# Optimization experiments

Measured on AMD Instinct MI355X. Metric: run time of the kernel, lower is better.

Reference implementation:

```python
import jax, jax.numpy as jnp
import numpy as np

B, T = 64, 1024
EMB = 10          # embedding_dim
H = 64            # hidden_size
NH = 2            # attention heads
IN = 3 * EMB      # 30 = GRU input_size
GAMMA = 1.0


def rbf(d):
    # BondExpansionRBF: exp(-gamma * |center - d|^2), centers = 1..10
    centers = jnp.arange(1, EMB + 1, dtype=d.dtype)          # [10]
    return jnp.exp(-GAMMA * (centers - d[..., None]) ** 2)   # [..., 10]


def gru_layer(x, w_ih, w_hh, b_ih, b_hh):
    # x: [B,T,D] -> [B,T,H]; torch GRU gate order: r, z, n
    Bn = x.shape[0]
    Hn = w_hh.shape[1]
    xw = jnp.einsum('btd,gd->btg', x, w_ih) + b_ih           # [B,T,3H] precomputed input proj

    def step(h, xt):
        gh = h @ w_hh.T + b_hh
        xr, xz, xn = jnp.split(xt, 3, axis=-1)
        hr, hz, hn = jnp.split(gh, 3, axis=-1)
        r = jax.nn.sigmoid(xr + hr)
        z = jax.nn.sigmoid(xz + hz)
        n = jnp.tanh(xn + r * hn)
        h = (1.0 - z) * n + z * h
        return h, h

    _, ys = jax.lax.scan(step, jnp.zeros((Bn, Hn), x.dtype), jnp.swapaxes(xw, 0, 1))
    return jnp.swapaxes(ys, 0, 1)


def mha(x, in_w, in_b, out_w, out_b):
    # torch nn.MultiheadAttention (batch_first, self-attn), eval mode
    Bn, Tn, E = x.shape
    Hd = E // NH
    qkv = x @ in_w.T + in_b                                   # [B,T,3E]
    q, k, v = jnp.split(qkv, 3, axis=-1)

    def heads(t):
        return t.reshape(Bn, Tn, NH, Hd).transpose(0, 2, 1, 3)  # [B,NH,T,Hd]

    q, k, v = heads(q), heads(k), heads(v)
    scores = jnp.einsum('bhqd,bhkd->bhqk', q, k) / jnp.asarray(np.sqrt(Hd), x.dtype)
    a = jax.nn.softmax(scores, axis=-1)
    o = jnp.einsum('bhqk,bhkd->bhqd', a, v).transpose(0, 2, 1, 3).reshape(Bn, Tn, E)
    return o @ out_w.T + out_b


def forward(atom_idx, bond_dist, emb, w_ih0, w_hh0, b_ih0, b_hh0,
            w_ih1, w_hh1, b_ih1, b_hh1, in_w1, in_b1, out_w1, out_b1,
            in_w2, in_b2, out_w2, out_b2, w_l, b_l, w_l1, b_l1):
    idx_i = atom_idx[..., 0]
    idx_j = atom_idx[..., 1]
    # index 0 -> zero vector (padding semantics of the python-loop conditionals)
    e_i = jnp.where((idx_i != 0)[..., None], emb[idx_i], 0.0)   # [B,T,10]
    e_j = jnp.where((idx_j != 0)[..., None], emb[idx_j], 0.0)   # [B,T,10]
    d = jnp.where((idx_i != 0)[..., None], rbf(bond_dist), 0.0)  # [B,T,10]
    x = jnp.concatenate([e_i, e_j, d], axis=-1)                  # [B,T,30]

    g = gru_layer(x, w_ih0, w_hh0, b_ih0, b_hh0)
    g = gru_layer(g, w_ih1, w_hh1, b_ih1, b_hh1)
    a = mha(g, in_w1, in_b1, out_w1, out_b1)
    a = mha(a, in_w2, in_b2, out_w2, out_b2)

    last = a[:, -1, :]                                           # [B,H]
    h = jax.nn.relu(last @ w_l.T + b_l)                          # [B,32]
    out = h @ w_l1.T + b_l1                                      # [B,1]
    return out[:, 0]                                             # [B]


def setup_inputs() -> dict:
    key = jax.random.key(0)
    ks = jax.random.split(key, 20)

    def n(k, shape, s=0.05):
        return jax.random.normal(k, shape, jnp.float32) * s

    return {
        'atom_idx': jax.random.randint(ks[0], (B, T, 2), 0, 119),
        'bond_dist': jax.random.uniform(ks[1], (B, T), jnp.float32) * 10.0,
        'emb': n(ks[2], (119, EMB), 1.0),
        'w_ih0': n(ks[3], (3 * H, IN)), 'w_hh0': n(ks[4], (3 * H, H)),
        'b_ih0': n(ks[5], (3 * H,)), 'b_hh0': n(ks[6], (3 * H,)),
        'w_ih1': n(ks[7], (3 * H, H)), 'w_hh1': n(ks[8], (3 * H, H)),
        'b_ih1': n(ks[9], (3 * H,)), 'b_hh1': n(ks[10], (3 * H,)),
        'in_w1': n(ks[11], (3 * H, H)), 'in_b1': n(ks[12], (3 * H,)),
        'out_w1': n(ks[13], (H, H)), 'out_b1': jnp.zeros((H,), jnp.float32),
        'in_w2': n(ks[14], (3 * H, H)), 'in_b2': n(ks[15], (3 * H,)),
        'out_w2': n(ks[16], (H, H)), 'out_b2': jnp.zeros((H,), jnp.float32),
        'w_l': n(ks[17], (32, H)), 'b_l': jnp.zeros((32,), jnp.float32),
        'w_l1': n(ks[18], (1, 32)), 'b_l1': jnp.zeros((1,), jnp.float32),
    }


def reference(atom_idx, bond_dist, emb, w_ih0, w_hh0, b_ih0, b_hh0,
              w_ih1, w_hh1, b_ih1, b_hh1, in_w1, in_b1, out_w1, out_b1,
              in_w2, in_b2, out_w2, out_b2, w_l, b_l, w_l1, b_l1):
    return forward(atom_idx, bond_dist, emb, w_ih0, w_hh0, b_ih0, b_hh0,
                   w_ih1, w_hh1, b_ih1, b_hh1, in_w1, in_b1, out_w1, out_b1,
                   in_w2, in_b2, out_w2, out_b2, w_l, b_l, w_l1, b_l1)
```

## Files before the change

### kernel.cpp

```cpp
#include <hip/hip_runtime.h>

typedef unsigned int uint_t;
typedef float v2f __attribute__((ext_vector_type(2)));

#define BB 64
#define TT 1024

__device__ __forceinline__ float sigm(float x) { return 1.f / (1.f + __expf(-x)); }
__device__ __forceinline__ float tanh_f(float x) { float e = __expf(2.f * x); return 1.f - 2.f / (e + 1.f); }
__device__ __forceinline__ int finitef(float x) { return (x == x) && (fabsf(x) < 1e30f); }

__device__ __forceinline__ void spinwait(volatile int* f, int v) {
  if (*f >= v) { asm volatile("" ::: "memory"); return; }
  int it = 0;
  while (*f < v && it < (1 << 15)) { __builtin_amdgcn_s_sleep(1); ++it; }
  asm volatile("" ::: "memory");
}

__device__ __forceinline__ float feat(int b, int t, int j,
                                      const int* atom_idx, const float* bond_dist,
                                      const float* emb) {
  int ii = atom_idx[(b * TT + t) * 2 + 0];
  if (j < 10) {
    return ii ? emb[ii * 10 + j] : 0.f;
  } else if (j < 20) {
    int jj = atom_idx[(b * TT + t) * 2 + 1];
    return jj ? emb[jj * 10 + (j - 10)] : 0.f;
  } else {
    float d = bond_dist[b * TT + t];
    float c = (float)(j - 19);
    float df = c - d;
    return ii ? __expf(-df * df) : 0.f;
  }
}

extern "C" __global__ void __launch_bounds__(256)
k_xw0(const int* atom_idx, const float* bond_dist, const float* emb,
      const float* w_ih0, const float* b_ih0, float* xw0) {
  int b  = blockIdx.x >> 4;
  int t0 = (blockIdx.x & 15) << 6;
  int tid = threadIdx.x;
  __shared__ float xt[64 * 31];
  for (int i = tid; i < 64 * 30; i += 256) {
    int r = i / 30, j = i % 30;
    xt[r * 31 + j] = feat(b, t0 + r, j, atom_idx, bond_dist, emb);
  }
  __syncthreads();
  int r = tid & 63, gq = tid >> 6;
  const float* ar = &xt[r * 31];
  for (int g0 = gq * 8; g0 < 192; g0 += 32) {
    float acc[8];
    #pragma unroll
    for (int j = 0; j < 8; ++j) acc[j] = b_ih0[g0 + j];
    #pragma unroll
    for (int c = 0; c < 30; ++c) {
      float a = ar[c];
      #pragma unroll
      for (int j = 0; j < 8; ++j) acc[j] += a * w_ih0[(g0 + j) * 30 + c];
    }
    #pragma unroll
    for (int j = 0; j < 8; ++j)
      xw0[((size_t)b * TT + t0 + r) * 192 + g0 + j] = acc[j];
  }
}

__device__ __forceinline__ void gemm64b(const float* __restrict__ act_g,
                                        const float* __restrict__ w,
                                        const float* __restrict__ bias,
                                        float* al,
                                        int G, int tid,
                                        float* out, int out_rstride, size_t out_base) {
  for (int i = tid; i < 64 * 64; i += 256) {
    int r = i >> 6, c = i & 63;
    al[r * 65 + c] = act_g[r * 64 + c];
  }
  __syncthreads();
  int r = tid & 63, gq = tid >> 6;
  const float* ar = &al[r * 65];
  for (int g0 = gq * 8; g0 < G; g0 += 32) {
    float acc[8];
    #pragma unroll
    for (int j = 0; j < 8; ++j) acc[j] = bias[g0 + j];
    #pragma unroll
    for (int c = 0; c < 64; ++c) {
      float a = ar[c];
      #pragma unroll
      for (int j = 0; j < 8; ++j) acc[j] += a * w[(size_t)(g0 + j) * 64 + c];
    }
    #pragma unroll
    for (int j = 0; j < 8; ++j)
      out[out_base + (size_t)r * out_rstride + g0 + j] = acc[j];
  }
}

__device__ __forceinline__ void loadw2(const float* p, v2f* w2) {
  const float4* p4 = (const float4*)p;
  #pragma unroll
  for (int i = 0; i < 16; ++i) {
    float4 a = p4[i];
    v2f lo; lo.x = a.x; lo.y = a.y;
    v2f hi; hi.x = a.z; hi.y = a.w;
    w2[2 * i] = lo; w2[2 * i + 1] = hi;
  }
}

extern "C" __global__ void __launch_bounds__(192, 1)
k_grufused(const float* xw0, const float* w_hh0, const float* b_hh0,
           const float* w_ih1, const float* b_ih1,
           const float* w_hh1, const float* b_hh1, float* g1out) {
  int b    = blockIdx.x;
  int lane = threadIdx.x & 63;
  int wid  = threadIdx.x >> 6;
  __shared__ __align__(16) float h0ring[16][64];
  __shared__ __align__(16) float xwring[16][192];
  __shared__ __align__(16) float h1pp[2][64];
  __shared__ int flags[3];

  if (threadIdx.x < 3) flags[threadIdx.x] = -1;
  if (wid == 0) h0ring[15][lane] = 0.f;
  if (wid == 2) h1pp[0][lane] = 0.f;
  __syncthreads();

  volatile int* w0d = &flags[0];
  volatile int* w1d = &flags[1];
  volatile int* w2d = &flags[2];

  if (wid == 0) {
    v2f wr2[32], wz2[32], wn2[32];
    loadw2(w_hh0 + (size_t)lane * 64,        wr2);
    loadw2(w_hh0 + (size_t)(64 + lane) * 64, wz2);
    loadw2(w_hh0 + (size_t)(128 + lane) * 64, wn2);
    float br = b_hh0[lane], bz = b_hh0[64 + lane], bn = b_hh0[128 + lane];
    float hv = 0.f;
    const float* xwb = xw0 + (size_t)b * TT * 192;
    float xr0 = xwb[      lane], xz0 = xwb[ 64 + lane], xn0 = xwb[128 + lane];
    float xr1 = xwb[192 + lane], xz1 = xwb[256 + lane], xn1 = xwb[320 + lane];
    float xr2 = xwb[384 + lane], xz2 = xwb[448 + lane], xn2 = xwb[512 + lane];
    float xr3 = xwb[576 + lane], xz3 = xwb[640 + lane], xn3 = xwb[704 + lane];

    auto gstep = [&](int s, float xr, float xz, float xn) {
      const float4* hp4 = (const float4*)h0ring[(s + 15) & 15];
      v2f ar; ar.x = br; ar.y = 0.f;
      v2f az; az.x = bz; az.y = 0.f;
      v2f an; an.x = bn; an.y = 0.f;
      #pragma unroll
      for (int i = 0; i < 16; ++i) {
        float4 h4 = hp4[i];
        v2f hlo; hlo.x = h4.x; hlo.y = h4.y;
        v2f hhi; hhi.x = h4.z; hhi.y = h4.w;
        ar += wr2[2*i] * hlo; ar += wr2[2*i+1] * hhi;
        az += wz2[2*i] * hlo; az += wz2[2*i+1] * hhi;
        an += wn2[2*i] * hlo; an += wn2[2*i+1] * hhi;
      }
      float r = sigm(xr + (ar.x + ar.y));
      float z = sigm(xz + (az.x + az.y));
      float n = tanh_f(xn + r * (an.x + an.y));
      hv = (1.f - z) * n + z * hv;
      h0ring[s & 15][lane] = hv;
    };
    auto pf = [&](int s, float& a, float& bb_, float& c) {
      const float* xp = xwb + (size_t)s * 192;
      a = xp[lane]; bb_ = xp[64 + lane]; c = xp[128 + lane];
    };

    for (int s0 = 0; s0 < TT; s0 += 4) {
      if (s0 >= 16) spinwait(w1d, s0 - 13);
      bool dopf = (s0 < TT - 4);
      gstep(s0 + 0, xr0, xz0, xn0); if (dopf) pf(s0 + 4, xr0, xz0, xn0);
      gstep(s0 + 1, xr1, xz1, xn1); if (dopf) pf(s0 + 5, xr1, xz1, xn1);
      gstep(s0 + 2, xr2, xz2, xn2); if (dopf) pf(s0 + 6, xr2, xz2, xn2);
      gstep(s0 + 3, xr3, xz3, xn3); if (dopf) pf(s0 + 7, xr3, xz3, xn3);
      asm volatile("" ::: "memory");
      if (lane == 0) *w0d = s0 + 3;
    }
  } else if (wid == 1) {
    v2f wr2[32], wz2[32], wn2[32];
    loadw2(w_ih1 + (size_t)lane * 64,        wr2);
    loadw2(w_ih1 + (size_t)(64 + lane) * 64, wz2);
    loadw2(w_ih1 + (size_t)(128 + lane) * 64, wn2);
    float br = b_ih1[lane], bz = b_ih1[64 + lane], bn = b_ih1[128 + lane];

    for (int t0 = 0; t0 < TT; t0 += 4) {
      spinwait(w0d, t0 + 3);
      if (t0 >= 16) spinwait(w2d, t0 - 13);
      #pragma unroll
      for (int k = 0; k < 4; ++k) {
        int t = t0 + k;
        const float4* hp4 = (const float4*)h0ring[t & 15];
        v2f ar; ar.x = br; ar.y = 0.f;
        v2f az; az.x = bz; az.y = 0.f;
        v2f an; an.x = bn; an.y = 0.f;
        #pragma unroll
        for (int i = 0; i < 16; ++i) {
          float4 h4 = hp4[i];
          v2f hlo; hlo.x = h4.x; hlo.y = h4.y;
          v2f hhi; hhi.x = h4.z; hhi.y = h4.w;
          ar += wr2[2*i] * hlo; ar += wr2[2*i+1] * hhi;
          az += wz2[2*i] * hlo; az += wz2[2*i+1] * hhi;
          an += wn2[2*i] * hlo; an += wn2[2*i+1] * hhi;
        }
        xwring[t & 15][lane]       = ar.x + ar.y;
        xwring[t & 15][64 + lane]  = az.x + az.y;
        xwring[t & 15][128 + lane] = an.x + an.y;
      }
      asm volatile("" ::: "memory");
      if (lane == 0) *w1d = t0 + 3;
    }
  } else {
    v2f wr2[32], wz2[32], wn2[32];
    loadw2(w_hh1 + (size_t)lane * 64,        wr2);
    loadw2(w_hh1 + (size_t)(64 + lane) * 64, wz2);
    loadw2(w_hh1 + (size_t)(128 + lane) * 64, wn2);
    float br = b_hh1[lane], bz = b_hh1[64 + lane], bn = b_hh1[128 + lane];
    float hv = 0.f;
    float* houtb = g1out + (size_t)b * TT * 64 + lane;

    for (int t0 = 0; t0 < TT; t0 += 4) {
      spinwait(w1d, t0 + 3);
      #pragma unroll
      for (int k = 0; k < 4; ++k) {
        int t = t0 + k;
        float xr = xwring[t & 15][lane];
        float xz = xwring[t & 15][64 + lane];
        float xn = xwring[t & 15][128 + lane];
        const float4* hp4 = (const float4*)h1pp[t & 1];
        v2f ar; ar.x = br; ar.y = 0.f;
        v2f az; az.x = bz; az.y = 0.f;
        v2f an; an.x = bn; an.y = 0.f;
        #pragma unroll
        for (int i = 0; i < 16; ++i) {
          float4 h4 = hp4[i];
          v2f hlo; hlo.x = h4.x; hlo.y = h4.y;
          v2f hhi; hhi.x = h4.z; hhi.y = h4.w;
          ar += wr2[2*i] * hlo; ar += wr2[2*i+1] * hhi;
          az += wz2[2*i] * hlo; az += wz2[2*i+1] * hhi;
          an += wn2[2*i] * hlo; an += wn2[2*i+1] * hhi;
        }
        float r = sigm(xr + (ar.x + ar.y));
        float z = sigm(xz + (az.x + az.y));
        float n = tanh_f(xn + r * (an.x + an.y));
        hv = (1.f - z) * n + z * hv;
        h1pp[(t + 1) & 1][lane] = hv;
        houtb[(size_t)t * 64] = hv;
      }
      asm volatile("" ::: "memory");
      if (lane == 0) *w2d = t0 + 3;
    }
  }
}

extern "C" __global__ void __launch_bounds__(256)
k_qkv(const float* g1, const float* in_w1, const float* in_b1,
      float* q1, float* k1, float* v1) {
  int b  = blockIdx.x >> 4;
  int t0 = (blockIdx.x & 15) << 6;
  int tid = threadIdx.x;
  __shared__ float al[64 * 65];
  const float* act = g1 + ((size_t)b * TT + t0) * 64;
  for (int i = tid; i < 64 * 64; i += 256) {
    int r = i >> 6, c = i & 63;
    al[r * 65 + c] = act[r * 64 + c];
  }
  __syncthreads();
  int r = tid & 63, gq = tid >> 6;
  const float* ar = &al[r * 65];
  for (int g0 = gq * 8; g0 < 192; g0 += 32) {
    float acc[8];
    #pragma unroll
    for (int j = 0; j < 8; ++j) acc[j] = in_b1[g0 + j];
    #pragma unroll
    for (int c = 0; c < 64; ++c) {
      float a = ar[c];
      #pragma unroll
      for (int j = 0; j < 8; ++j) acc[j] += a * in_w1[(size_t)(g0 + j) * 64 + c];
    }
    int p = g0 / 64;
    float* outp = (p == 0) ? q1 : ((p == 1) ? k1 : v1);
    #pragma unroll
    for (int j = 0; j < 8; ++j) {
      int rem = (g0 - p * 64) + j;
      int hd = rem >> 5, d = rem & 31;
      outp[(((size_t)b * 2 + hd) * TT + t0 + r) * 32 + d] = acc[j];
    }
  }
}

extern "C" __global__ void __launch_bounds__(256, 2)
k_attn(const float* q1, const float* k1, const float* v1, float* po, float* ml) {
  int gid = blockIdx.x;
  int b   = gid >> 3;
  int h   = (gid >> 2) & 1;
  int seg = (gid >> 1) & 1;
  int qb  = gid & 1;
  int tid = threadIdx.x;
  int tq0 = qb * 512 + tid;
  __shared__ __align__(16) float Kt[64 * 32];
  __shared__ __align__(16) float Vt[64 * 32];
  v2f q2[32], o2[32];
  const float* qp0 = q1 + (((size_t)b * 2 + h) * TT + tq0) * 32;
  const float* qp1 = qp0 + 256 * 32;
  #pragma unroll
  for (int i = 0; i < 8; ++i) {
    float4 v0 = ((const float4*)qp0)[i];
    float4 v1r = ((const float4*)qp1)[i];
    q2[4*i+0] = (v2f){v0.x, v1r.x};
    q2[4*i+1] = (v2f){v0.y, v1r.y};
    q2[4*i+2] = (v2f){v0.z, v1r.z};
    q2[4*i+3] = (v2f){v0.w, v1r.w};
  }
  #pragma unroll
  for (int i = 0; i < 32; ++i) o2[i] = (v2f){0.f, 0.f};
  float m0 = -1e30f, l0 = 0.f, m1 = -1e30f, l1 = 0.f;
  const float scale = 0.17677669529663687f;
  const float4* kb = (const float4*)(k1 + ((size_t)b * 2 + h) * TT * 32);
  const float4* vb = (const float4*)(v1 + ((size_t)b * 2 + h) * TT * 32);
  int k0 = seg << 9;
  for (int kt = k0; kt < k0 + 512; kt += 64) {
    __syncthreads();
    ((float4*)Kt)[tid]       = kb[kt * 8 + tid];
    ((float4*)Kt)[tid + 256] = kb[kt * 8 + tid + 256];
    ((float4*)Vt)[tid]       = vb[kt * 8 + tid];
    ((float4*)Vt)[tid + 256] = vb[kt * 8 + tid + 256];
    __syncthreads();
    #pragma unroll 1
    for (int c0 = 0; c0 < 64; c0 += 8) {
      v2f sv2[8];
      #pragma unroll
      for (int j = 0; j < 8; ++j) {
        const float4* kr = (const float4*)&Kt[(c0 + j) * 32];
        v2f a0 = (v2f){0.f, 0.f}, a1 = (v2f){0.f, 0.f};
        #pragma unroll
        for (int i = 0; i < 8; ++i) {
          float4 kv = kr[i];
          a0 += q2[4*i+0] * (v2f){kv.x, kv.x};
          a1 += q2[4*i+1] * (v2f){kv.y, kv.y};
          a0 += q2[4*i+2] * (v2f){kv.z, kv.z};
          a1 += q2[4*i+3] * (v2f){kv.w, kv.w};
        }
        v2f s = a0 + a1;
        sv2[j] = (v2f){s.x * scale, s.y * scale};
      }
      float cm0 = sv2[0].x, cm1 = sv2[0].y;
      #pragma unroll
      for (int j = 1; j < 8; ++j) { cm0 = fmaxf(cm0, sv2[j].x); cm1 = fmaxf(cm1, sv2[j].y); }
      float mn0 = fmaxf(m0, cm0), mn1 = fmaxf(m1, cm1);
      float al0 = __expf(m0 - mn0), al1 = __expf(m1 - mn1);
      float ps0 = 0.f, ps1 = 0.f;
      #pragma unroll
      for (int j = 0; j < 8; ++j) {
        float e0 = __expf(sv2[j].x - mn0); ps0 += e0;
        float e1 = __expf(sv2[j].y - mn1); ps1 += e1;
        sv2[j] = (v2f){e0, e1};
      }
      l0 = l0 * al0 + ps0; m0 = mn0;
      l1 = l1 * al1 + ps1; m1 = mn1;
      v2f al2 = (v2f){al0, al1};
      #pragma unroll
      for (int i = 0; i < 8; ++i) {
        v2f A0 = o2[4*i+0] * al2;
        v2f A1 = o2[4*i+1] * al2;
        v2f A2 = o2[4*i+2] * al2;
        v2f A3 = o2[4*i+3] * al2;
        #pragma unroll
        for (int j = 0; j < 8; ++j) {
          float4 vv = *(const float4*)&Vt[(c0 + j) * 32 + 4 * i];
          A0 += sv2[j] * (v2f){vv.x, vv.x};
          A1 += sv2[j] * (v2f){vv.y, vv.y};
          A2 += sv2[j] * (v2f){vv.z, vv.z};
          A3 += sv2[j] * (v2f){vv.w, vv.w};
        }
        o2[4*i+0] = A0; o2[4*i+1] = A1; o2[4*i+2] = A2; o2[4*i+3] = A3;
      }
    }
  }
  size_t rb0 = (((size_t)(b * 2 + h)) * 2 + seg) * TT + tq0;
  size_t rb1 = rb0 + 256;
  float* op0 = po + rb0 * 32;
  float* op1 = po + rb1 * 32;
  #pragma unroll
  for (int i = 0; i < 8; ++i) {
    float4 s0; s0.x = o2[4*i+0].x; s0.y = o2[4*i+1].x; s0.z = o2[4*i+2].x; s0.w = o2[4*i+3].x;
    float4 s1; s1.x = o2[4*i+0].y; s1.y = o2[4*i+1].y; s1.z = o2[4*i+2].y; s1.w = o2[4*i+3].y;
    ((float4*)op0)[i] = s0;
    ((float4*)op1)[i] = s1;
  }
  ml[rb0 * 2 + 0] = m0; ml[rb0 * 2 + 1] = l0;
  ml[rb1 * 2 + 0] = m1; ml[rb1 * 2 + 1] = l1;
}

extern "C" __global__ void __launch_bounds__(256)
k_attn_comb(const float* po, const float* ml, float* attnO) {
  int row = blockIdx.x * 256 + threadIdx.x;
  int bh = row >> 10;
  int t  = row & 1023;
  int b = bh >> 1, h = bh & 1;
  size_t r0 = ((size_t)bh * 2 + 0) * TT + t;
  size_t r1 = ((size_t)bh * 2 + 1) * TT + t;
  float m0 = ml[r0 * 2], l0 = ml[r0 * 2 + 1];
  float m1 = ml[r1 * 2], l1 = ml[r1 * 2 + 1];
  float m = fmaxf(m0, m1);
  float w0 = __expf(m0 - m), w1 = __expf(m1 - m);
  float inv = 1.f / (w0 * l0 + w1 * l1);
  w0 *= inv; w1 *= inv;
  const float4* p0 = (const float4*)(po + r0 * 32);
  const float4* p1 = (const float4*)(po + r1 * 32);
  float* op = attnO + ((size_t)b * TT + t) * 64 + h * 32;
  #pragma unroll
  for (int i = 0; i < 8; ++i) {
    float4 a = p0[i], c = p1[i], r;
    r.x = a.x * w0 + c.x * w1; r.y = a.y * w0 + c.y * w1;
    r.z = a.z * w0 + c.z * w1; r.w = a.w * w0 + c.w * w1;
    ((float4*)op)[i] = r;
  }
}

extern "C" __global__ void __launch_bounds__(256)
k_oproj(const float* attnO, const float* out_w1, const float* out_b1, float* a1) {
  int b  = blockIdx.x >> 4;
  int t0 = (blockIdx.x & 15) << 6;
  __shared__ float al[64 * 65];
  gemm64b(attnO + ((size_t)b * TT + t0) * 64, out_w1, out_b1, al, 64, threadIdx.x,
          a1, 64, ((size_t)b * TT + t0) * 64);
}

extern "C" __global__ void __launch_bounds__(256)
k_mha2kv(const float* a1, const float* in_w2, const float* in_b2,
         float* s2, float* v2) {
  int b  = blockIdx.x >> 4;
  int t0 = (blockIdx.x & 15) << 6;
  int tid = threadIdx.x;
  __shared__ float a1r[64 * 65];
  __shared__ float q2s[64];
  __shared__ float alast[64];
  if (tid < 64) alast[tid] = a1[((size_t)b * TT + (TT - 1)) * 64 + tid];
  for (int i = tid; i < 4096; i += 256) {
    int r = i >> 6, e = i & 63;
    a1r[r * 65 + e] = a1[((size_t)b * TT + t0 + r) * 64 + e];
  }
  __syncthreads();
  if (tid < 64) {
    float acc = in_b2[tid];
    const float* wr = in_w2 + (size_t)tid * 64;
    #pragma unroll
    for (int e = 0; e < 64; ++e) acc += alast[e] * wr[e];
    q2s[tid] = acc;
  }
  __syncthreads();
  int tt = tid & 63;
  int role = tid >> 6;
  const float* ar = &a1r[tt * 65];
  const float scale = 0.17677669529663687f;
  if (role < 2) {
    float s = 0.f;
    for (int d = 0; d < 32; ++d) {
      int row = 64 + role * 32 + d;
      const float* wr = in_w2 + (size_t)row * 64;
      float acc = in_b2[row];
      #pragma unroll
      for (int e = 0; e < 64; ++e) acc += ar[e] * wr[e];
      s += q2s[row - 64] * acc;
    }
    s2[((size_t)b * 2 + role) * TT + t0 + tt] = s * scale;
  } else {
    int half = role - 2;
    for (int d = 0; d < 32; ++d) {
      int vd = half * 32 + d;
      int row = 128 + vd;
      const float* wr = in_w2 + (size_t)row * 64;
      float acc = in_b2[row];
      #pragma unroll
      for (int e = 0; e < 64; ++e) acc += ar[e] * wr[e];
      v2[((size_t)b * TT + t0 + tt) * 64 + vd] = acc;
    }
  }
}

extern "C" __global__ void __launch_bounds__(256)
k_final(const float* s2, const float* v2,
        const float* out_w2, const float* out_b2,
        const float* w_l, const float* b_l,
        const float* w_l1, const float* b_l1,
        float* out) {
  int b = blockIdx.x;
  int tid = threadIdx.x;
  __shared__ float sm[2 * 1024];
  __shared__ float red[8];
  __shared__ float invl[2];
  __shared__ float opart[4 * 64];
  __shared__ float of[64];
  __shared__ float a2[64];
  __shared__ float hbuf[32];
  __shared__ int bad;
  if (tid == 0) bad = 0;
  for (int i = tid; i < 2048; i += 256) sm[i] = s2[(size_t)b * 2 * TT + i];
  __syncthreads();
  int lane = tid & 63;
  int wid = tid >> 6;
  for (int hh = 0; hh < 2; ++hh) {
    float mx = -1e30f;
    for (int i = tid; i < 1024; i += 256) mx = fmaxf(mx, sm[hh * 1024 + i]);
    #pragma unroll
    for (int off = 32; off > 0; off >>= 1) mx = fmaxf(mx, __shfl_down(mx, off));
    if (lane == 0) red[wid] = mx;
    __syncthreads();
    if (tid == 0) red[4] = fmaxf(fmaxf(red[0], red[1]), fmaxf(red[2], red[3]));
    __syncthreads();
    mx = red[4];
    float s = 0.f;
    for (int i = tid; i < 1024; i += 256) {
      float e = __expf(sm[hh * 1024 + i] - mx);
      sm[hh * 1024 + i] = e;
      s += e;
    }
    #pragma unroll
    for (int off = 32; off > 0; off >>= 1) s += __shfl_down(s, off);
    if (lane == 0) red[wid] = s;
    __syncthreads();
    if (tid == 0) invl[hh] = 1.f / (red[0] + red[1] + red[2] + red[3]);
    __syncthreads();
  }
  {
    int dp = tid & 63;
    int part = tid >> 6;
    int hh = dp >> 5;
    float acc = 0.f;
    for (int t = part * 256; t < part * 256 + 256; ++t)
      acc += sm[hh * 1024 + t] * v2[((size_t)b * TT + t) * 64 + dp];
    opart[part * 64 + dp] = acc;
  }
  __syncthreads();
  if (tid < 64) {
    float o = (opart[tid] + opart[64 + tid] + opart[128 + tid] + opart[192 + tid]) * invl[tid >> 5];
    of[tid] = o;
    if (!finitef(o)) bad = 1;
  }
  __syncthreads();
  if (tid < 64) {
    float acc = out_b2[tid];
    const float* wr = out_w2 + (size_t)tid * 64;
    #pragma unroll
    for (int d = 0; d < 64; ++d) acc += of[d] * wr[d];
    a2[tid] = acc;
  }
  __syncthreads();
  if (tid < 32) {
    float acc = b_l[tid];
    const float* wr = w_l + (size_t)tid * 64;
    #pragma unroll
    for (int e = 0; e < 64; ++e) acc += a2[e] * wr[e];
    hbuf[tid] = fmaxf(acc, 0.f);
  }
  __syncthreads();
  if (tid == 0) {
    float acc = b_l1[0];
    #pragma unroll
    for (int j = 0; j < 32; ++j) acc += hbuf[j] * w_l1[j];
    out[b] = bad ? 777.0f : acc;
  }
}

extern "C" void kernel_launch(void* const* d_in, const int* in_sizes, int n_in,
                              void* d_out, int out_size, void* d_ws, size_t ws_size,
                              hipStream_t stream) {
  const int*   atom_idx  = (const int*)d_in[0];
  const float* bond_dist = (const float*)d_in[1];
  const float* emb       = (const float*)d_in[2];
  const float* w_ih0     = (const float*)d_in[3];
  const float* w_hh0     = (const float*)d_in[4];
  const float* b_ih0     = (const float*)d_in[5];
  const float* b_hh0     = (const float*)d_in[6];
  const float* w_ih1     = (const float*)d_in[7];
  const float* w_hh1     = (const float*)d_in[8];
  const float* b_ih1     = (const float*)d_in[9];
  const float* b_hh1     = (const float*)d_in[10];
  const float* in_w1     = (const float*)d_in[11];
  const float* in_b1     = (const float*)d_in[12];
  const float* out_w1    = (const float*)d_in[13];
  const float* out_b1    = (const float*)d_in[14];
  const float* in_w2     = (const float*)d_in[15];
  const float* in_b2     = (const float*)d_in[16];
  const float* out_w2    = (const float*)d_in[17];
  const float* out_b2    = (const float*)d_in[18];
  const float* w_l       = (const float*)d_in[19];
  const float* b_l       = (const float*)d_in[20];
  const float* w_l1      = (const float*)d_in[21];
  const float* b_l1      = (const float*)d_in[22];

  char* ws = (char*)d_ws;
  float* X  = (float*)(ws);
  float* A  = (float*)(ws + 50331648);
  float* Bq = (float*)(ws + 67108864);
  float* D  = (float*)(ws + 83886080);
  float* q1 = X;
  float* k1 = X + 4194304;
  float* v1 = X + 8388608;
  float* po = (float*)(ws + 16777216);
  float* ml = Bq;

  k_xw0      <<<dim3(1024), dim3(256), 0, stream>>>(atom_idx, bond_dist, emb, w_ih0, b_ih0, X);
  k_grufused <<<dim3(64),   dim3(192), 0, stream>>>(X, w_hh0, b_hh0, w_ih1, b_ih1, w_hh1, b_hh1, Bq);
  k_qkv      <<<dim3(1024), dim3(256), 0, stream>>>(Bq, in_w1, in_b1, q1, k1, v1);
  k_attn     <<<dim3(512),  dim3(256), 0, stream>>>(q1, k1, v1, po, ml);
  k_attn_comb<<<dim3(512),  dim3(256), 0, stream>>>(po, ml, A);
  k_oproj    <<<dim3(1024), dim3(256), 0, stream>>>(A, out_w1, out_b1, Bq);
  k_mha2kv   <<<dim3(1024), dim3(256), 0, stream>>>(Bq, in_w2, in_b2, D, X);
  k_final    <<<dim3(64),   dim3(256), 0, stream>>>(D, X, out_w2, out_b2, w_l, b_l, w_l1, b_l1, (float*)d_out);
}
```

Measured before the change: 1.301 ms.

## Process four query rows per thread in attention kernel to double K/V reuse

The attention kernel now assigns four query rows per thread instead of two and halves the grid, so each K/V tile loaded into shared memory is reused across twice as many queries. This cuts LDS reads and global K/V traffic per query. In exchange, per-thread register use roughly doubles, launch bounds drop to one block per SM, and there are fewer blocks to hide latency, risking spills or lower occupancy.

```diff
diff --git a/kernel.cpp b/kernel.cpp
--- a/kernel.cpp
+++ b/kernel.cpp
@@ -285,32 +285,34 @@
   }
 }
 
-extern "C" __global__ void __launch_bounds__(256, 2)
+extern "C" __global__ void __launch_bounds__(256, 1)
 k_attn(const float* q1, const float* k1, const float* v1, float* po, float* ml) {
   int gid = blockIdx.x;
-  int b   = gid >> 3;
-  int h   = (gid >> 2) & 1;
-  int seg = (gid >> 1) & 1;
-  int qb  = gid & 1;
+  int b   = gid >> 2;
+  int h   = (gid >> 1) & 1;
+  int seg = gid & 1;
   int tid = threadIdx.x;
-  int tq0 = qb * 512 + tid;
   __shared__ __align__(16) float Kt[64 * 32];
   __shared__ __align__(16) float Vt[64 * 32];
-  v2f q2[32], o2[32];
-  const float* qp0 = q1 + (((size_t)b * 2 + h) * TT + tq0) * 32;
-  const float* qp1 = qp0 + 256 * 32;
+  v2f qA[32], oA[32], qB[32], oB[32];
+  {
+    const float* p0 = q1 + (((size_t)b * 2 + h) * TT + tid) * 32;
+    #pragma unroll
+    for (int i = 0; i < 8; ++i) {
+      float4 a = ((const float4*)(p0))[i];
+      float4 c = ((const float4*)(p0 + 256 * 32))[i];
+      float4 d = ((const float4*)(p0 + 512 * 32))[i];
+      float4 e = ((const float4*)(p0 + 768 * 32))[i];
+      qA[4*i+0] = (v2f){a.x, c.x}; qA[4*i+1] = (v2f){a.y, c.y};
+      qA[4*i+2] = (v2f){a.z, c.z}; qA[4*i+3] = (v2f){a.w, c.w};
+      qB[4*i+0] = (v2f){d.x, e.x}; qB[4*i+1] = (v2f){d.y, e.y};
+      qB[4*i+2] = (v2f){d.z, e.z}; qB[4*i+3] = (v2f){d.w, e.w};
+    }
+  }
   #pragma unroll
-  for (int i = 0; i < 8; ++i) {
-    float4 v0 = ((const float4*)qp0)[i];
-    float4 v1r = ((const float4*)qp1)[i];
-    q2[4*i+0] = (v2f){v0.x, v1r.x};
-    q2[4*i+1] = (v2f){v0.y, v1r.y};
-    q2[4*i+2] = (v2f){v0.z, v1r.z};
-    q2[4*i+3] = (v2f){v0.w, v1r.w};
-  }
-  #pragma unroll
-  for (int i = 0; i < 32; ++i) o2[i] = (v2f){0.f, 0.f};
+  for (int i = 0; i < 32; ++i) { oA[i] = (v2f){0.f, 0.f}; oB[i] = (v2f){0.f, 0.f}; }
   float m0 = -1e30f, l0 = 0.f, m1 = -1e30f, l1 = 0.f;
+  float m2 = -1e30f, l2 = 0.f, m3 = -1e30f, l3 = 0.f;
   const float scale = 0.17677669529663687f;
   const float4* kb = (const float4*)(k1 + ((size_t)b * 2 + h) * TT * 32);
   const float4* vb = (const float4*)(v1 + ((size_t)b * 2 + h) * TT * 32);
@@ -324,68 +326,90 @@
     __syncthreads();
     #pragma unroll 1
     for (int c0 = 0; c0 < 64; c0 += 8) {
-      v2f sv2[8];
+      v2f svA[8], svB[8];
       #pragma unroll
       for (int j = 0; j < 8; ++j) {
         const float4* kr = (const float4*)&Kt[(c0 + j) * 32];
-        v2f a0 = (v2f){0.f, 0.f}, a1 = (v2f){0.f, 0.f};
+        v2f aA = (v2f){0.f, 0.f}, bA = (v2f){0.f, 0.f};
+        v2f aB = (v2f){0.f, 0.f}, bB = (v2f){0.f, 0.f};
         #pragma unroll
         for (int i = 0; i < 8; ++i) {
           float4 kv = kr[i];
-          a0 += q2[4*i+0] * (v2f){kv.x, kv.x};
-          a1 += q2[4*i+1] * (v2f){kv.y, kv.y};
-          a0 += q2[4*i+2] * (v2f){kv.z, kv.z};
-          a1 += q2[4*i+3] * (v2f){kv.w, kv.w};
+          v2f kx = (v2f){kv.x, kv.x}, ky = (v2f){kv.y, kv.y};
+          v2f kz = (v2f){kv.z, kv.z}, kw = (v2f){kv.w, kv.w};
+          aA += qA[4*i+0] * kx; bA += qA[4*i+1] * ky;
+          aA += qA[4*i+2] * kz; bA += qA[4*i+3] * kw;
+          aB += qB[4*i+0] * kx; bB += qB[4*i+1] * ky;
+          aB += qB[4*i+2] * kz; bB += qB[4*i+3] * kw;
         }
-        v2f s = a0 + a1;
-        sv2[j] = (v2f){s.x * scale, s.y * scale};
+        v2f sA = aA + bA, sB = aB + bB;
+        svA[j] = (v2f){sA.x * scale, sA.y * scale};
+        svB[j] = (v2f){sB.x * scale, sB.y * scale};
       }
-      float cm0 = sv2[0].x, cm1 = sv2[0].y;
-      #pragma unroll
-      for (int j = 1; j < 8; ++j) { cm0 = fmaxf(cm0, sv2[j].x); cm1 = fmaxf(cm1, sv2[j].y); }
+      float cm0 = svA[0].x, cm1 = svA[0].y, cm2 = svB[0].x, cm3 = svB[0].y;
+      #pragma unroll
+      for (int j = 1; j < 8; ++j) {
+        cm0 = fmaxf(cm0, svA[j].x); cm1 = fmaxf(cm1, svA[j].y);
+        cm2 = fmaxf(cm2, svB[j].x); cm3 = fmaxf(cm3, svB[j].y);
+      }
       float mn0 = fmaxf(m0, cm0), mn1 = fmaxf(m1, cm1);
+      float mn2 = fmaxf(m2, cm2), mn3 = fmaxf(m3, cm3);
       float al0 = __expf(m0 - mn0), al1 = __expf(m1 - mn1);
-      float ps0 = 0.f, ps1 = 0.f;
+      float al2 = __expf(m2 - mn2), al3 = __expf(m3 - mn3);
+      float ps0 = 0.f, ps1 = 0.f, ps2 = 0.f, ps3 = 0.f;
       #pragma unroll
       for (int j = 0; j < 8; ++j) {
-        float e0 = __expf(sv2[j].x - mn0); ps0 += e0;
-        float e1 = __expf(sv2[j].y - mn1); ps1 += e1;
-        sv2[j] = (v2f){e0, e1};
+        float e0 = __expf(svA[j].x - mn0); ps0 += e0;
+        float e1 = __expf(svA[j].y - mn1); ps1 += e1;
+        float e2 = __expf(svB[j].x - mn2); ps2 += e2;
+        float e3 = __expf(svB[j].y - mn3); ps3 += e3;
+        svA[j] = (v2f){e0, e1};
+        svB[j] = (v2f){e2, e3};
       }
       l0 = l0 * al0 + ps0; m0 = mn0;
       l1 = l1 * al1 + ps1; m1 = mn1;
-      v2f al2 = (v2f){al0, al1};
+      l2 = l2 * al2 + ps2; m2 = mn2;
+      l3 = l3 * al3 + ps3; m3 = mn3;
+      v2f alA = (v2f){al0, al1}, alB = (v2f){al2, al3};
       #pragma unroll
       for (int i = 0; i < 8; ++i) {
-        v2f A0 = o2[4*i+0] * al2;
-        v2f A1 = o2[4*i+1] * al2;
-        v2f A2 = o2[4*i+2] * al2;
-        v2f A3 = o2[4*i+3] * al2;
+        v2f A0 = oA[4*i+0] * alA, A1 = oA[4*i+1] * alA;
+        v2f A2 = oA[4*i+2] * alA, A3 = oA[4*i+3] * alA;
+        v2f B0 = oB[4*i+0] * alB, B1 = oB[4*i+1] * alB;
+        v2f B2 = oB[4*i+2] * alB, B3 = oB[4*i+3] * alB;
         #pragma unroll
         for (int j = 0; j < 8; ++j) {
           float4 vv = *(const float4*)&Vt[(c0 + j) * 32 + 4 * i];
-          A0 += sv2[j] * (v2f){vv.x, vv.x};
-          A1 += sv2[j] * (v2f){vv.y, vv.y};
-          A2 += sv2[j] * (v2f){vv.z, vv.z};
-          A3 += sv2[j] * (v2f){vv.w, vv.w};
+          v2f vx = (v2f){vv.x, vv.x}, vy = (v2f){vv.y, vv.y};
+          v2f vz = (v2f){vv.z, vv.z}, vw = (v2f){vv.w, vv.w};
+          A0 += svA[j] * vx; A1 += svA[j] * vy; A2 += svA[j] * vz; A3 += svA[j] * vw;
+          B0 += svB[j] * vx; B1 += svB[j] * vy; B2 += svB[j] * vz; B3 += svB[j] * vw;
         }
-        o2[4*i+0] = A0; o2[4*i+1] = A1; o2[4*i+2] = A2; o2[4*i+3] = A3;
+        oA[4*i+0] = A0; oA[4*i+1] = A1; oA[4*i+2] = A2; oA[4*i+3] = A3;
+        oB[4*i+0] = B0; oB[4*i+1] = B1; oB[4*i+2] = B2; oB[4*i+3] = B3;
       }
     }
   }
-  size_t rb0 = (((size_t)(b * 2 + h)) * 2 + seg) * TT + tq0;
-  size_t rb1 = rb0 + 256;
-  float* op0 = po + rb0 * 32;
-  float* op1 = po + rb1 * 32;
+  size_t rb = (((size_t)(b * 2 + h)) * 2 + seg) * TT + tid;
+  float* op0 = po + rb * 32;
+  float* op1 = po + (rb + 256) * 32;
+  float* op2 = po + (rb + 512) * 32;
+  float* op3 = po + (rb + 768) * 32;
   #pragma unroll
   for (int i = 0; i < 8; ++i) {
-    float4 s0; s0.x = o2[4*i+0].x; s0.y = o2[4*i+1].x; s0.z = o2[4*i+2].x; s0.w = o2[4*i+3].x;
-    float4 s1; s1.x = o2[4*i+0].y; s1.y = o2[4*i+1].y; s1.z = o2[4*i+2].y; s1.w = o2[4*i+3].y;
+    float4 s0; s0.x = oA[4*i+0].x; s0.y = oA[4*i+1].x; s0.z = oA[4*i+2].x; s0.w = oA[4*i+3].x;
+    float4 s1; s1.x = oA[4*i+0].y; s1.y = oA[4*i+1].y; s1.z = oA[4*i+2].y; s1.w = oA[4*i+3].y;
+    float4 s2; s2.x = oB[4*i+0].x; s2.y = oB[4*i+1].x; s2.z = oB[4*i+2].x; s2.w = oB[4*i+3].x;
+    float4 s3; s3.x = oB[4*i+0].y; s3.y = oB[4*i+1].y; s3.z = oB[4*i+2].y; s3.w = oB[4*i+3].y;
     ((float4*)op0)[i] = s0;
     ((float4*)op1)[i] = s1;
-  }
-  ml[rb0 * 2 + 0] = m0; ml[rb0 * 2 + 1] = l0;
-  ml[rb1 * 2 + 0] = m1; ml[rb1 * 2 + 1] = l1;
+    ((float4*)op2)[i] = s2;
+    ((float4*)op3)[i] = s3;
+  }
+  ml[rb * 2 + 0] = m0;           ml[rb * 2 + 1] = l0;
+  ml[(rb + 256) * 2 + 0] = m1;   ml[(rb + 256) * 2 + 1] = l1;
+  ml[(rb + 512) * 2 + 0] = m2;   ml[(rb + 512) * 2 + 1] = l2;
+  ml[(rb + 768) * 2 + 0] = m3;   ml[(rb + 768) * 2 + 1] = l3;
 }
 
 extern "C" __global__ void __launch_bounds__(256)
@@ -600,7 +624,7 @@
   k_xw0      <<<dim3(1024), dim3(256), 0, stream>>>(atom_idx, bond_dist, emb, w_ih0, b_ih0, X);
   k_grufused <<<dim3(64),   dim3(192), 0, stream>>>(X, w_hh0, b_hh0, w_ih1, b_ih1, w_hh1, b_hh1, Bq);
   k_qkv      <<<dim3(1024), dim3(256), 0, stream>>>(Bq, in_w1, in_b1, q1, k1, v1);
-  k_attn     <<<dim3(512),  dim3(256), 0, stream>>>(q1, k1, v1, po, ml);
+  k_attn     <<<dim3(256),  dim3(256), 0, stream>>>(q1, k1, v1, po, ml);
   k_attn_comb<<<dim3(512),  dim3(256), 0, stream>>>(po, ml, A);
   k_oproj    <<<dim3(1024), dim3(256), 0, stream>>>(A, out_w1, out_b1, Bq);
   k_mha2kv   <<<dim3(1024), dim3(256), 0, stream>>>(Bq, in_w2, in_b2, D, X);
```

After: 1.445 ms. +11.1%, slower.

## Split attention into two sequential key-segment launches with in-place merge

Applied to the files above, without the earlier changes.

Replaces the single attention kernel, which had each thread handle two query rows over one key half, with two launches of a one-query-per-thread kernel. Each launch covers one key segment, and the second launch merges its result with the first using log-sum-exp weights. This removes the separate combine kernel and the packed v2f math, and the output projection now reads the per-head layout directly. In exchange it adds a launch, gives up the v2f packed FMAs, and runs only one half of the keys per launch, so parallelism within each launch is lower.

```diff
diff --git a/kernel.cpp b/kernel.cpp
--- a/kernel.cpp
+++ b/kernel.cpp
@@ -61,35 +61,6 @@
     #pragma unroll
     for (int j = 0; j < 8; ++j)
       xw0[((size_t)b * TT + t0 + r) * 192 + g0 + j] = acc[j];
-  }
-}
-
-__device__ __forceinline__ void gemm64b(const float* __restrict__ act_g,
-                                        const float* __restrict__ w,
-                                        const float* __restrict__ bias,
-                                        float* al,
-                                        int G, int tid,
-                                        float* out, int out_rstride, size_t out_base) {
-  for (int i = tid; i < 64 * 64; i += 256) {
-    int r = i >> 6, c = i & 63;
-    al[r * 65 + c] = act_g[r * 64 + c];
-  }
-  __syncthreads();
-  int r = tid & 63, gq = tid >> 6;
-  const float* ar = &al[r * 65];
-  for (int g0 = gq * 8; g0 < G; g0 += 32) {
-    float acc[8];
-    #pragma unroll
-    for (int j = 0; j < 8; ++j) acc[j] = bias[g0 + j];
-    #pragma unroll
-    for (int c = 0; c < 64; ++c) {
-      float a = ar[c];
-      #pragma unroll
-      for (int j = 0; j < 8; ++j) acc[j] += a * w[(size_t)(g0 + j) * 64 + c];
-    }
-    #pragma unroll
-    for (int j = 0; j < 8; ++j)
-      out[out_base + (size_t)r * out_rstride + g0 + j] = acc[j];
   }
 }
 
@@ -285,32 +256,27 @@
   }
 }
 
-extern "C" __global__ void __launch_bounds__(256, 2)
-k_attn(const float* q1, const float* k1, const float* v1, float* po, float* ml) {
+extern "C" __global__ void __launch_bounds__(256)
+k_attn_seg(const float* q1, const float* k1, const float* v1,
+           float* po, float* L0buf, int seg) {
   int gid = blockIdx.x;
   int b   = gid >> 3;
   int h   = (gid >> 2) & 1;
-  int seg = (gid >> 1) & 1;
-  int qb  = gid & 1;
+  int qb  = gid & 3;
   int tid = threadIdx.x;
-  int tq0 = qb * 512 + tid;
+  int tq  = qb * 256 + tid;
   __shared__ __align__(16) float Kt[64 * 32];
   __shared__ __align__(16) float Vt[64 * 32];
-  v2f q2[32], o2[32];
-  const float* qp0 = q1 + (((size_t)b * 2 + h) * TT + tq0) * 32;
-  const float* qp1 = qp0 + 256 * 32;
+  float q[32], o[32];
+  const float* qp = q1 + (((size_t)b * 2 + h) * TT + tq) * 32;
   #pragma unroll
   for (int i = 0; i < 8; ++i) {
-    float4 v0 = ((const float4*)qp0)[i];
-    float4 v1r = ((const float4*)qp1)[i];
-    q2[4*i+0] = (v2f){v0.x, v1r.x};
-    q2[4*i+1] = (v2f){v0.y, v1r.y};
-    q2[4*i+2] = (v2f){v0.z, v1r.z};
-    q2[4*i+3] = (v2f){v0.w, v1r.w};
+    float4 v = ((const float4*)qp)[i];
+    q[4 * i] = v.x; q[4 * i + 1] = v.y; q[4 * i + 2] = v.z; q[4 * i + 3] = v.w;
   }
   #pragma unroll
-  for (int i = 0; i < 32; ++i) o2[i] = (v2f){0.f, 0.f};
-  float m0 = -1e30f, l0 = 0.f, m1 = -1e30f, l1 = 0.f;
+  for (int i = 0; i < 32; ++i) o[i] = 0.f;
+  float m = -1e30f, l = 0.f;
   const float scale = 0.17677669529663687f;
   const float4* kb = (const float4*)(k1 + ((size_t)b * 2 + h) * TT * 32);
   const float4* vb = (const float4*)(v1 + ((size_t)b * 2 + h) * TT * 32);
@@ -324,103 +290,105 @@
     __syncthreads();
     #pragma unroll 1
     for (int c0 = 0; c0 < 64; c0 += 8) {
-      v2f sv2[8];
+      float sv[8];
       #pragma unroll
       for (int j = 0; j < 8; ++j) {
         const float4* kr = (const float4*)&Kt[(c0 + j) * 32];
-        v2f a0 = (v2f){0.f, 0.f}, a1 = (v2f){0.f, 0.f};
+        float a0 = 0, a1 = 0, a2 = 0, a3 = 0;
         #pragma unroll
         for (int i = 0; i < 8; ++i) {
           float4 kv = kr[i];
-          a0 += q2[4*i+0] * (v2f){kv.x, kv.x};
-          a1 += q2[4*i+1] * (v2f){kv.y, kv.y};
-          a0 += q2[4*i+2] * (v2f){kv.z, kv.z};
-          a1 += q2[4*i+3] * (v2f){kv.w, kv.w};
+          a0 += q[4 * i] * kv.x; a1 += q[4 * i + 1] * kv.y;
+          a2 += q[4 * i + 2] * kv.z; a3 += q[4 * i + 3] * kv.w;
         }
-        v2f s = a0 + a1;
-        sv2[j] = (v2f){s.x * scale, s.y * scale};
+        sv[j] = ((a0 + a1) + (a2 + a3)) * scale;
       }
-      float cm0 = sv2[0].x, cm1 = sv2[0].y;
-      #pragma unroll
-      for (int j = 1; j < 8; ++j) { cm0 = fmaxf(cm0, sv2[j].x); cm1 = fmaxf(cm1, sv2[j].y); }
-      float mn0 = fmaxf(m0, cm0), mn1 = fmaxf(m1, cm1);
-      float al0 = __expf(m0 - mn0), al1 = __expf(m1 - mn1);
-      float ps0 = 0.f, ps1 = 0.f;
-      #pragma unroll
-      for (int j = 0; j < 8; ++j) {
-        float e0 = __expf(sv2[j].x - mn0); ps0 += e0;
-        float e1 = __expf(sv2[j].y - mn1); ps1 += e1;
-        sv2[j] = (v2f){e0, e1};
-      }
-      l0 = l0 * al0 + ps0; m0 = mn0;
-      l1 = l1 * al1 + ps1; m1 = mn1;
-      v2f al2 = (v2f){al0, al1};
+      float cm = sv[0];
+      #pragma unroll
+      for (int j = 1; j < 8; ++j) cm = fmaxf(cm, sv[j]);
+      float mnew = fmaxf(m, cm);
+      float alpha = __expf(m - mnew);
+      float ps = 0.f;
+      #pragma unroll
+      for (int j = 0; j < 8; ++j) { sv[j] = __expf(sv[j] - mnew); ps += sv[j]; }
+      l = l * alpha + ps;
+      m = mnew;
       #pragma unroll
       for (int i = 0; i < 8; ++i) {
-        v2f A0 = o2[4*i+0] * al2;
-        v2f A1 = o2[4*i+1] * al2;
-        v2f A2 = o2[4*i+2] * al2;
-        v2f A3 = o2[4*i+3] * al2;
+        float4 acc;
+        acc.x = o[4 * i] * alpha; acc.y = o[4 * i + 1] * alpha;
+        acc.z = o[4 * i + 2] * alpha; acc.w = o[4 * i + 3] * alpha;
         #pragma unroll
         for (int j = 0; j < 8; ++j) {
           float4 vv = *(const float4*)&Vt[(c0 + j) * 32 + 4 * i];
-          A0 += sv2[j] * (v2f){vv.x, vv.x};
-          A1 += sv2[j] * (v2f){vv.y, vv.y};
-          A2 += sv2[j] * (v2f){vv.z, vv.z};
-          A3 += sv2[j] * (v2f){vv.w, vv.w};
+          acc.x += sv[j] * vv.x; acc.y += sv[j] * vv.y;
+          acc.z += sv[j] * vv.z; acc.w += sv[j] * vv.w;
         }
-        o2[4*i+0] = A0; o2[4*i+1] = A1; o2[4*i+2] = A2; o2[4*i+3] = A3;
+        o[4 * i] = acc.x; o[4 * i + 1] = acc.y; o[4 * i + 2] = acc.z; o[4 * i + 3] = acc.w;
       }
     }
   }
-  size_t rb0 = (((size_t)(b * 2 + h)) * 2 + seg) * TT + tq0;
-  size_t rb1 = rb0 + 256;
-  float* op0 = po + rb0 * 32;
-  float* op1 = po + rb1 * 32;
-  #pragma unroll
-  for (int i = 0; i < 8; ++i) {
-    float4 s0; s0.x = o2[4*i+0].x; s0.y = o2[4*i+1].x; s0.z = o2[4*i+2].x; s0.w = o2[4*i+3].x;
-    float4 s1; s1.x = o2[4*i+0].y; s1.y = o2[4*i+1].y; s1.z = o2[4*i+2].y; s1.w = o2[4*i+3].y;
-    ((float4*)op0)[i] = s0;
-    ((float4*)op1)[i] = s1;
-  }
-  ml[rb0 * 2 + 0] = m0; ml[rb0 * 2 + 1] = l0;
-  ml[rb1 * 2 + 0] = m1; ml[rb1 * 2 + 1] = l1;
+  size_t row = ((size_t)(b * 2 + h)) * TT + tq;
+  float* op = po + row * 32;
+  if (seg == 0) {
+    float invl = 1.f / l;
+    #pragma unroll
+    for (int i = 0; i < 8; ++i) {
+      float4 s4; s4.x = o[4*i] * invl; s4.y = o[4*i+1] * invl;
+      s4.z = o[4*i+2] * invl; s4.w = o[4*i+3] * invl;
+      ((float4*)op)[i] = s4;
+    }
+    L0buf[row] = m + logf(l);
+  } else {
+    float L0 = L0buf[row];
+    float L1 = m + logf(l);
+    float M  = fmaxf(L0, L1);
+    float w0 = __expf(L0 - M), w1 = __expf(L1 - M);
+    float inv = 1.f / (w0 + w1);
+    w0 *= inv;
+    w1 *= inv / l;
+    #pragma unroll
+    for (int i = 0; i < 8; ++i) {
+      float4 p0 = ((const float4*)op)[i];
+      float4 s4;
+      s4.x = w0 * p0.x + w1 * o[4*i];
+      s4.y = w0 * p0.y + w1 * o[4*i+1];
+      s4.z = w0 * p0.z + w1 * o[4*i+2];
+      s4.w = w0 * p0.w + w1 * o[4*i+3];
+      ((float4*)op)[i] = s4;
+    }
+  }
 }
 
 extern "C" __global__ void __launch_bounds__(256)
-k_attn_comb(const float* po, const float* ml, float* attnO) {
-  int row = blockIdx.x * 256 + threadIdx.x;
-  int bh = row >> 10;
-  int t  = row & 1023;
-  int b = bh >> 1, h = bh & 1;
-  size_t r0 = ((size_t)bh * 2 + 0) * TT + t;
-  size_t r1 = ((size_t)bh * 2 + 1) * TT + t;
-  float m0 = ml[r0 * 2], l0 = ml[r0 * 2 + 1];
-  float m1 = ml[r1 * 2], l1 = ml[r1 * 2 + 1];
-  float m = fmaxf(m0, m1);
-  float w0 = __expf(m0 - m), w1 = __expf(m1 - m);
-  float inv = 1.f / (w0 * l0 + w1 * l1);
-  w0 *= inv; w1 *= inv;
-  const float4* p0 = (const float4*)(po + r0 * 32);
-  const float4* p1 = (const float4*)(po + r1 * 32);
-  float* op = attnO + ((size_t)b * TT + t) * 64 + h * 32;
-  #pragma unroll
-  for (int i = 0; i < 8; ++i) {
-    float4 a = p0[i], c = p1[i], r;
-    r.x = a.x * w0 + c.x * w1; r.y = a.y * w0 + c.y * w1;
-    r.z = a.z * w0 + c.z * w1; r.w = a.w * w0 + c.w * w1;
-    ((float4*)op)[i] = r;
-  }
-}
-
-extern "C" __global__ void __launch_bounds__(256)
-k_oproj(const float* attnO, const float* out_w1, const float* out_b1, float* a1) {
+k_oproj(const float* paired, const float* out_w1, const float* out_b1, float* a1) {
   int b  = blockIdx.x >> 4;
   int t0 = (blockIdx.x & 15) << 6;
+  int tid = threadIdx.x;
   __shared__ float al[64 * 65];
-  gemm64b(attnO + ((size_t)b * TT + t0) * 64, out_w1, out_b1, al, 64, threadIdx.x,
-          a1, 64, ((size_t)b * TT + t0) * 64);
+  const float* p0 = paired + ((size_t)(b * 2 + 0) * TT + t0) * 32;
+  const float* p1 = paired + ((size_t)(b * 2 + 1) * TT + t0) * 32;
+  for (int i = tid; i < 64 * 64; i += 256) {
+    int r = i >> 6, c = i & 63;
+    al[r * 65 + c] = (c < 32) ? p0[r * 32 + c] : p1[r * 32 + (c - 32)];
+  }
+  __syncthreads();
+  int r = tid & 63, gq = tid >> 6;
+  const float* ar = &al[r * 65];
+  for (int g0 = gq * 8; g0 < 64; g0 += 32) {
+    float acc[8];
+    #pragma unroll
+    for (int j = 0; j < 8; ++j) acc[j] = out_b1[g0 + j];
+    #pragma unroll
+    for (int c = 0; c < 64; ++c) {
+      float a = ar[c];
+      #pragma unroll
+      for (int j = 0; j < 8; ++j) acc[j] += a * out_w1[(size_t)(g0 + j) * 64 + c];
+    }
+    #pragma unroll
+    for (int j = 0; j < 8; ++j)
+      a1[((size_t)b * TT + t0 + r) * 64 + g0 + j] = acc[j];
+  }
 }
 
 extern "C" __global__ void __launch_bounds__(256)
@@ -594,14 +562,12 @@
   float* q1 = X;
   float* k1 = X + 4194304;
   float* v1 = X + 8388608;
-  float* po = (float*)(ws + 16777216);
-  float* ml = Bq;
 
   k_xw0      <<<dim3(1024), dim3(256), 0, stream>>>(atom_idx, bond_dist, emb, w_ih0, b_ih0, X);
   k_grufused <<<dim3(64),   dim3(192), 0, stream>>>(X, w_hh0, b_hh0, w_ih1, b_ih1, w_hh1, b_hh1, Bq);
   k_qkv      <<<dim3(1024), dim3(256), 0, stream>>>(Bq, in_w1, in_b1, q1, k1, v1);
-  k_attn     <<<dim3(512),  dim3(256), 0, stream>>>(q1, k1, v1, po, ml);
-  k_attn_comb<<<dim3(512),  dim3(256), 0, stream>>>(po, ml, A);
+  k_attn_seg <<<dim3(512),  dim3(256), 0, stream>>>(q1, k1, v1, A, D, 0);
+  k_attn_seg <<<dim3(512),  dim3(256), 0, stream>>>(q1, k1, v1, A, D, 1);
   k_oproj    <<<dim3(1024), dim3(256), 0, stream>>>(A, out_w1, out_b1, Bq);
   k_mha2kv   <<<dim3(1024), dim3(256), 0, stream>>>(Bq, in_w2, in_b2, D, X);
   k_final    <<<dim3(64),   dim3(256), 0, stream>>>(D, X, out_w2, out_b2, w_l, b_l, w_l1, b_l1, (float*)d_out);
```

Result: slower. 1.501 ms (+15.3%).

## Fold attention segment combine into sequential two-pass attention kernel launches

Applied to the files above, without the earlier changes.

The separate attention-combine kernel is removed. Attention now runs as two launches, one per key segment. The first writes normalized partial output plus a log-sum-exp. The second reads those back, merges its own partial result in place, and writes a head-interleaved buffer that the output projection reads directly. This drops one kernel launch and the intermediate m/l buffer, but each attention launch has only half the blocks and the two segments now run one after the other instead of concurrently.

```diff
diff --git a/kernel.cpp b/kernel.cpp
--- a/kernel.cpp
+++ b/kernel.cpp
@@ -61,35 +61,6 @@
     #pragma unroll
     for (int j = 0; j < 8; ++j)
       xw0[((size_t)b * TT + t0 + r) * 192 + g0 + j] = acc[j];
-  }
-}
-
-__device__ __forceinline__ void gemm64b(const float* __restrict__ act_g,
-                                        const float* __restrict__ w,
-                                        const float* __restrict__ bias,
-                                        float* al,
-                                        int G, int tid,
-                                        float* out, int out_rstride, size_t out_base) {
-  for (int i = tid; i < 64 * 64; i += 256) {
-    int r = i >> 6, c = i & 63;
-    al[r * 65 + c] = act_g[r * 64 + c];
-  }
-  __syncthreads();
-  int r = tid & 63, gq = tid >> 6;
-  const float* ar = &al[r * 65];
-  for (int g0 = gq * 8; g0 < G; g0 += 32) {
-    float acc[8];
-    #pragma unroll
-    for (int j = 0; j < 8; ++j) acc[j] = bias[g0 + j];
-    #pragma unroll
-    for (int c = 0; c < 64; ++c) {
-      float a = ar[c];
-      #pragma unroll
-      for (int j = 0; j < 8; ++j) acc[j] += a * w[(size_t)(g0 + j) * 64 + c];
-    }
-    #pragma unroll
-    for (int j = 0; j < 8; ++j)
-      out[out_base + (size_t)r * out_rstride + g0 + j] = acc[j];
   }
 }
 
@@ -286,11 +257,11 @@
 }
 
 extern "C" __global__ void __launch_bounds__(256, 2)
-k_attn(const float* q1, const float* k1, const float* v1, float* po, float* ml) {
+k_attn_seg(const float* q1, const float* k1, const float* v1,
+           float* po, float* L0buf, int seg) {
   int gid = blockIdx.x;
-  int b   = gid >> 3;
-  int h   = (gid >> 2) & 1;
-  int seg = (gid >> 1) & 1;
+  int b   = gid >> 2;
+  int h   = (gid >> 1) & 1;
   int qb  = gid & 1;
   int tid = threadIdx.x;
   int tq0 = qb * 512 + tid;
@@ -373,54 +344,82 @@
       }
     }
   }
-  size_t rb0 = (((size_t)(b * 2 + h)) * 2 + seg) * TT + tq0;
-  size_t rb1 = rb0 + 256;
-  float* op0 = po + rb0 * 32;
-  float* op1 = po + rb1 * 32;
-  #pragma unroll
-  for (int i = 0; i < 8; ++i) {
-    float4 s0; s0.x = o2[4*i+0].x; s0.y = o2[4*i+1].x; s0.z = o2[4*i+2].x; s0.w = o2[4*i+3].x;
-    float4 s1; s1.x = o2[4*i+0].y; s1.y = o2[4*i+1].y; s1.z = o2[4*i+2].y; s1.w = o2[4*i+3].y;
-    ((float4*)op0)[i] = s0;
-    ((float4*)op1)[i] = s1;
-  }
-  ml[rb0 * 2 + 0] = m0; ml[rb0 * 2 + 1] = l0;
-  ml[rb1 * 2 + 0] = m1; ml[rb1 * 2 + 1] = l1;
+  size_t row0 = ((size_t)(b * 2 + h)) * TT + tq0;
+  size_t row1 = row0 + 256;
+  float* op0 = po + row0 * 32;
+  float* op1 = po + row1 * 32;
+  if (seg == 0) {
+    float i0 = 1.f / l0, i1 = 1.f / l1;
+    #pragma unroll
+    for (int i = 0; i < 8; ++i) {
+      float4 s0; s0.x = o2[4*i+0].x * i0; s0.y = o2[4*i+1].x * i0;
+      s0.z = o2[4*i+2].x * i0; s0.w = o2[4*i+3].x * i0;
+      float4 s1; s1.x = o2[4*i+0].y * i1; s1.y = o2[4*i+1].y * i1;
+      s1.z = o2[4*i+2].y * i1; s1.w = o2[4*i+3].y * i1;
+      ((float4*)op0)[i] = s0;
+      ((float4*)op1)[i] = s1;
+    }
+    L0buf[row0] = m0 + logf(l0);
+    L0buf[row1] = m1 + logf(l1);
+  } else {
+    float L0a = L0buf[row0], L1a = m0 + logf(l0);
+    float Ma  = fmaxf(L0a, L1a);
+    float wa0 = __expf(L0a - Ma), wa1 = __expf(L1a - Ma);
+    float inva = 1.f / (wa0 + wa1);
+    wa0 *= inva; wa1 *= inva / l0;
+    float L0b = L0buf[row1], L1b = m1 + logf(l1);
+    float Mb  = fmaxf(L0b, L1b);
+    float wb0 = __expf(L0b - Mb), wb1 = __expf(L1b - Mb);
+    float invb = 1.f / (wb0 + wb1);
+    wb0 *= invb; wb1 *= invb / l1;
+    #pragma unroll
+    for (int i = 0; i < 8; ++i) {
+      float4 p0 = ((const float4*)op0)[i];
+      float4 p1 = ((const float4*)op1)[i];
+      float4 s0, s1;
+      s0.x = wa0 * p0.x + wa1 * o2[4*i+0].x;
+      s0.y = wa0 * p0.y + wa1 * o2[4*i+1].x;
+      s0.z = wa0 * p0.z + wa1 * o2[4*i+2].x;
+      s0.w = wa0 * p0.w + wa1 * o2[4*i+3].x;
+      s1.x = wb0 * p1.x + wb1 * o2[4*i+0].y;
+      s1.y = wb0 * p1.y + wb1 * o2[4*i+1].y;
+      s1.z = wb0 * p1.z + wb1 * o2[4*i+2].y;
+      s1.w = wb0 * p1.w + wb1 * o2[4*i+3].y;
+      ((float4*)op0)[i] = s0;
+      ((float4*)op1)[i] = s1;
+    }
+  }
 }
 
 extern "C" __global__ void __launch_bounds__(256)
-k_attn_comb(const float* po, const float* ml, float* attnO) {
-  int row = blockIdx.x * 256 + threadIdx.x;
-  int bh = row >> 10;
-  int t  = row & 1023;
-  int b = bh >> 1, h = bh & 1;
-  size_t r0 = ((size_t)bh * 2 + 0) * TT + t;
-  size_t r1 = ((size_t)bh * 2 + 1) * TT + t;
-  float m0 = ml[r0 * 2], l0 = ml[r0 * 2 + 1];
-  float m1 = ml[r1 * 2], l1 = ml[r1 * 2 + 1];
-  float m = fmaxf(m0, m1);
-  float w0 = __expf(m0 - m), w1 = __expf(m1 - m);
-  float inv = 1.f / (w0 * l0 + w1 * l1);
-  w0 *= inv; w1 *= inv;
-  const float4* p0 = (const float4*)(po + r0 * 32);
-  const float4* p1 = (const float4*)(po + r1 * 32);
-  float* op = attnO + ((size_t)b * TT + t) * 64 + h * 32;
-  #pragma unroll
-  for (int i = 0; i < 8; ++i) {
-    float4 a = p0[i], c = p1[i], r;
-    r.x = a.x * w0 + c.x * w1; r.y = a.y * w0 + c.y * w1;
-    r.z = a.z * w0 + c.z * w1; r.w = a.w * w0 + c.w * w1;
-    ((float4*)op)[i] = r;
-  }
-}
-
-extern "C" __global__ void __launch_bounds__(256)
-k_oproj(const float* attnO, const float* out_w1, const float* out_b1, float* a1) {
+k_oproj(const float* paired, const float* out_w1, const float* out_b1, float* a1) {
   int b  = blockIdx.x >> 4;
   int t0 = (blockIdx.x & 15) << 6;
+  int tid = threadIdx.x;
   __shared__ float al[64 * 65];
-  gemm64b(attnO + ((size_t)b * TT + t0) * 64, out_w1, out_b1, al, 64, threadIdx.x,
-          a1, 64, ((size_t)b * TT + t0) * 64);
+  const float* p0 = paired + ((size_t)(b * 2 + 0) * TT + t0) * 32;
+  const float* p1 = paired + ((size_t)(b * 2 + 1) * TT + t0) * 32;
+  for (int i = tid; i < 64 * 64; i += 256) {
+    int r = i >> 6, c = i & 63;
+    al[r * 65 + c] = (c < 32) ? p0[r * 32 + c] : p1[r * 32 + (c - 32)];
+  }
+  __syncthreads();
+  int r = tid & 63, gq = tid >> 6;
+  const float* ar = &al[r * 65];
+  for (int g0 = gq * 8; g0 < 64; g0 += 32) {
+    float acc[8];
+    #pragma unroll
+    for (int j = 0; j < 8; ++j) acc[j] = out_b1[g0 + j];
+    #pragma unroll
+    for (int c = 0; c < 64; ++c) {
+      float a = ar[c];
+      #pragma unroll
+      for (int j = 0; j < 8; ++j) acc[j] += a * out_w1[(size_t)(g0 + j) * 64 + c];
+    }
+    #pragma unroll
+    for (int j = 0; j < 8; ++j)
+      a1[((size_t)b * TT + t0 + r) * 64 + g0 + j] = acc[j];
+  }
 }
 
 extern "C" __global__ void __launch_bounds__(256)
@@ -594,14 +593,12 @@
   float* q1 = X;
   float* k1 = X + 4194304;
   float* v1 = X + 8388608;
-  float* po = (float*)(ws + 16777216);
-  float* ml = Bq;
 
   k_xw0      <<<dim3(1024), dim3(256), 0, stream>>>(atom_idx, bond_dist, emb, w_ih0, b_ih0, X);
   k_grufused <<<dim3(64),   dim3(192), 0, stream>>>(X, w_hh0, b_hh0, w_ih1, b_ih1, w_hh1, b_hh1, Bq);
   k_qkv      <<<dim3(1024), dim3(256), 0, stream>>>(Bq, in_w1, in_b1, q1, k1, v1);
-  k_attn     <<<dim3(512),  dim3(256), 0, stream>>>(q1, k1, v1, po, ml);
-  k_attn_comb<<<dim3(512),  dim3(256), 0, stream>>>(po, ml, A);
+  k_attn_seg <<<dim3(256),  dim3(256), 0, stream>>>(q1, k1, v1, A, D, 0);
+  k_attn_seg <<<dim3(256),  dim3(256), 0, stream>>>(q1, k1, v1, A, D, 1);
   k_oproj    <<<dim3(1024), dim3(256), 0, stream>>>(A, out_w1, out_b1, Bq);
   k_mha2kv   <<<dim3(1024), dim3(256), 0, stream>>>(Bq, in_w2, in_b2, D, X);
   k_final    <<<dim3(64),   dim3(256), 0, stream>>>(D, X, out_w2, out_b2, w_l, b_l, w_l1, b_l1, (float*)d_out);
```

Result: slower. 1.366 ms (+5.0%).
